# Optimization experiments

Measured on AMD Instinct MI355X. Metric: run time of the kernel, lower is better.

The kernel has to match this reference:

```python
import jax, jax.numpy as jnp
import numpy as np

VOCAB = 100000
EMB = 300
BATCH = 16384
TOTAL = 65536      # total ragged context tokens (avg 4 per instance)
NG_WORDS = 5


def setup_inputs() -> dict:
    key = jax.random.key(0)
    k1, k2, k3, k4, k5, k6 = jax.random.split(key, 6)
    # learned parameters: nn.Embedding weights, init uniform(-1, 1)
    W_in = jax.random.uniform(k1, (VOCAB, EMB), dtype=jnp.float32, minval=-1.0, maxval=1.0)
    W_out = jax.random.uniform(k2, (VOCAB, EMB), dtype=jnp.float32, minval=-1.0, maxval=1.0)
    # ragged batch flattened: indices + sorted segment ids (instance membership)
    flat_idx = jax.random.randint(k3, (TOTAL,), 0, VOCAB, dtype=jnp.int64)
    segment_ids = jnp.sort(jax.random.randint(k4, (TOTAL,), 0, BATCH, dtype=jnp.int64))
    out_idx = jax.random.randint(k5, (BATCH,), 0, VOCAB, dtype=jnp.int64)
    # forward_neg: multinomial over uniform dist == uniform randint over vocab
    ng_idx = jax.random.randint(k6, (BATCH * NG_WORDS,), 0, VOCAB, dtype=jnp.int64)
    return {"W_in": W_in, "W_out": W_out, "flat_idx": flat_idx,
            "segment_ids": segment_ids, "out_idx": out_idx, "ng_idx": ng_idx}


def reference(W_in, W_out, flat_idx, segment_ids, out_idx, ng_idx):
    # forward_in: per-instance sum of in-embedding rows (fused gather + segment_sum)
    in_vec = jax.ops.segment_sum(W_in[flat_idx], segment_ids, num_segments=BATCH)  # [B, EMB]
    # forward_out: plain embedding lookup
    out_vec = W_out[out_idx]                                                        # [B, EMB]
    # forward_neg: negative-sample embeddings, viewed [B, NG_WORDS, EMB]
    neg_vec = W_out[ng_idx].reshape(BATCH, NG_WORDS, EMB)
    return (in_vec, out_vec, neg_vec)
```

## Files before the change

kernel.cpp:

```cpp
#include <hip/hip_runtime.h>

#define VOCAB  100000
#define EMB    300
#define BATCH  16384
#define TOTAL  65536
#define NG     5
#define CHUNKS 75

__global__ __launch_bounds__(64) void segsum_kernel(
    const float* __restrict__ W_in,
    const int*   __restrict__ flat_idx,
    const int*   __restrict__ seg_ids,
    float*       __restrict__ in_vec)
{
    const int seg  = blockIdx.x;
    const int lane = threadIdx.x;

    int lo = 0, hi = TOTAL;
    while (lo < hi) { int mid = (lo + hi) >> 1; if (seg_ids[mid] < seg) lo = mid + 1; else hi = mid; }
    const int start = lo;
    hi = TOTAL;
    while (lo < hi) { int mid = (lo + hi) >> 1; if (seg_ids[mid] < seg + 1) lo = mid + 1; else hi = mid; }
    const int end = lo;

    float4 acc0 = make_float4(0.f, 0.f, 0.f, 0.f);
    float4 acc1 = make_float4(0.f, 0.f, 0.f, 0.f);
    const bool extra = lane < (CHUNKS - 64);

    for (int t = start; t < end; ++t) {
        const int idx = flat_idx[t];
        const float4* row = reinterpret_cast<const float4*>(W_in + (size_t)idx * EMB);
        const float4 v0 = row[lane];
        acc0.x += v0.x; acc0.y += v0.y; acc0.z += v0.z; acc0.w += v0.w;
        if (extra) {
            const float4 v1 = row[lane + 64];
            acc1.x += v1.x; acc1.y += v1.y; acc1.z += v1.z; acc1.w += v1.w;
        }
    }

    float4* dst = reinterpret_cast<float4*>(in_vec + (size_t)seg * EMB);
    dst[lane] = acc0;
    if (extra) dst[lane + 64] = acc1;
}

__global__ __launch_bounds__(256) void gather_kernel(
    const float* __restrict__ W_out,
    const int*   __restrict__ out_idx,
    const int*   __restrict__ ng_idx,
    float*       __restrict__ out_vec,
    float*       __restrict__ neg_vec)
{
    const int gid = blockIdx.x * blockDim.x + threadIdx.x;
    const int total_chunks = (BATCH + BATCH * NG) * CHUNKS;
    if (gid >= total_chunks) return;

    const int row = gid / CHUNKS;
    const int c   = gid % CHUNKS;

    int idx;
    float* dst;
    if (row < BATCH) {
        idx = out_idx[row];
        dst = out_vec + (size_t)row * EMB;
    } else {
        const int rr = row - BATCH;
        idx = ng_idx[rr];
        dst = neg_vec + (size_t)rr * EMB;
    }

    const float4* src = reinterpret_cast<const float4*>(W_out + (size_t)idx * EMB);
    reinterpret_cast<float4*>(dst)[c] = src[c];
}

extern "C" void kernel_launch(void* const* d_in, const int* in_sizes, int n_in,
                              void* d_out, int out_size, void* d_ws, size_t ws_size,
                              hipStream_t stream)
{
    const float* W_in   = (const float*)d_in[0];
    const float* W_out  = (const float*)d_in[1];
    const int*   flat   = (const int*)d_in[2];
    const int*   segids = (const int*)d_in[3];
    const int*   outidx = (const int*)d_in[4];
    const int*   ngidx  = (const int*)d_in[5];

    float* o       = (float*)d_out;
    float* in_vec  = o;
    float* out_vec = o + (size_t)BATCH * EMB;
    float* neg_vec = o + (size_t)2 * BATCH * EMB;

    segsum_kernel<<<BATCH, 64, 0, stream>>>(W_in, flat, segids, in_vec);

    const int total_chunks = (BATCH + BATCH * NG) * CHUNKS;
    const int threads = 256;
    const int blocks  = (total_chunks + threads - 1) / threads;
    gather_kernel<<<blocks, threads, 0, stream>>>(W_out, outidx, ngidx, out_vec, neg_vec);
}
```

Measured before the change: 73.01 us.

## Fuse segment-sum and gather into one interleaved kernel with ballot-based bounds search

Merges the segment-sum and the W_out gather into one launch. Every eighth block in the first span runs segment-sum work with four segments per block, and the other blocks copy gather chunks, so the two memory-bound workloads overlap on the device. The serial binary search is replaced by a three-level wavefront ballot search. Indices are loaded cooperatively and broadcast with shuffles, and outputs use nontemporal stores. This removes one launch and the serialized latency-bound search, at the cost of more complex block indexing and an uneven mix of work per block.

```diff
diff --git a/kernel.cpp b/kernel.cpp
--- a/kernel.cpp
+++ b/kernel.cpp
@@ -7,69 +7,90 @@
 #define NG     5
 #define CHUNKS 75
 
-__global__ __launch_bounds__(64) void segsum_kernel(
+#define NBLK_A 4096
+#define NBLK_B 28800
+#define NBLK   (NBLK_A + NBLK_B)
+#define A_SPAN (NBLK_A * 8)
+
+typedef float f4 __attribute__((ext_vector_type(4)));
+
+__device__ __forceinline__ int lb64(const int* __restrict__ seg, int v, int lane) {
+    int base = 0;
+    unsigned long long m;
+    int p = lane * 1024 + 1023;
+    m = __ballot(seg[p] < v);
+    base += (int)__popcll(m) << 10;
+    p = base + lane * 16 + 15;
+    m = __ballot((p < TOTAL) && (seg[p] < v));
+    base += (int)__popcll(m) << 4;
+    p = base + lane;
+    m = __ballot((lane < 16) && (p < TOTAL) && (seg[p] < v));
+    base += (int)__popcll(m);
+    return base;
+}
+
+__global__ __launch_bounds__(256) void fused_kernel(
     const float* __restrict__ W_in,
+    const float* __restrict__ W_out,
     const int*   __restrict__ flat_idx,
     const int*   __restrict__ seg_ids,
-    float*       __restrict__ in_vec)
-{
-    const int seg  = blockIdx.x;
-    const int lane = threadIdx.x;
-
-    int lo = 0, hi = TOTAL;
-    while (lo < hi) { int mid = (lo + hi) >> 1; if (seg_ids[mid] < seg) lo = mid + 1; else hi = mid; }
-    const int start = lo;
-    hi = TOTAL;
-    while (lo < hi) { int mid = (lo + hi) >> 1; if (seg_ids[mid] < seg + 1) lo = mid + 1; else hi = mid; }
-    const int end = lo;
-
-    float4 acc0 = make_float4(0.f, 0.f, 0.f, 0.f);
-    float4 acc1 = make_float4(0.f, 0.f, 0.f, 0.f);
-    const bool extra = lane < (CHUNKS - 64);
-
-    for (int t = start; t < end; ++t) {
-        const int idx = flat_idx[t];
-        const float4* row = reinterpret_cast<const float4*>(W_in + (size_t)idx * EMB);
-        const float4 v0 = row[lane];
-        acc0.x += v0.x; acc0.y += v0.y; acc0.z += v0.z; acc0.w += v0.w;
-        if (extra) {
-            const float4 v1 = row[lane + 64];
-            acc1.x += v1.x; acc1.y += v1.y; acc1.z += v1.z; acc1.w += v1.w;
-        }
-    }
-
-    float4* dst = reinterpret_cast<float4*>(in_vec + (size_t)seg * EMB);
-    dst[lane] = acc0;
-    if (extra) dst[lane + 64] = acc1;
-}
-
-__global__ __launch_bounds__(256) void gather_kernel(
-    const float* __restrict__ W_out,
     const int*   __restrict__ out_idx,
     const int*   __restrict__ ng_idx,
+    float*       __restrict__ in_vec,
     float*       __restrict__ out_vec,
     float*       __restrict__ neg_vec)
 {
-    const int gid = blockIdx.x * blockDim.x + threadIdx.x;
-    const int total_chunks = (BATCH + BATCH * NG) * CHUNKS;
-    if (gid >= total_chunks) return;
+    const unsigned bid = blockIdx.x;
 
-    const int row = gid / CHUNKS;
-    const int c   = gid % CHUNKS;
+    if (bid < A_SPAN && (bid & 7u) == 0u) {
+        const int aid  = (int)(bid >> 3);
+        const int wid  = threadIdx.x >> 6;
+        const int lane = threadIdx.x & 63;
+        const int seg  = aid * 4 + wid;
 
-    int idx;
-    float* dst;
-    if (row < BATCH) {
-        idx = out_idx[row];
-        dst = out_vec + (size_t)row * EMB;
+        const int start = lb64(seg_ids, seg,     lane);
+        const int end   = lb64(seg_ids, seg + 1, lane);
+
+        f4 acc0 = {0.f, 0.f, 0.f, 0.f};
+        f4 acc1 = {0.f, 0.f, 0.f, 0.f};
+        const bool extra = lane < (CHUNKS - 64);
+
+        for (int t0 = start; t0 < end; t0 += 64) {
+            const int n = min(64, end - t0);
+            const int myidx = (lane < n) ? flat_idx[t0 + lane] : 0;
+            for (int j = 0; j < n; ++j) {
+                const int idx = __shfl(myidx, j);
+                const f4* row = reinterpret_cast<const f4*>(W_in + (size_t)idx * EMB);
+                acc0 += row[lane];
+                if (extra) acc1 += row[lane + 64];
+            }
+        }
+
+        f4* dst = reinterpret_cast<f4*>(in_vec + (size_t)seg * EMB);
+        __builtin_nontemporal_store(acc0, dst + lane);
+        if (extra) __builtin_nontemporal_store(acc1, dst + lane + 64);
     } else {
-        const int rr = row - BATCH;
-        idx = ng_idx[rr];
-        dst = neg_vec + (size_t)rr * EMB;
+        const int b = (bid < A_SPAN) ? (int)(bid - (bid >> 3) - 1u)
+                                     : (int)(NBLK_A * 7 + (bid - A_SPAN));
+        const int gid = b * 256 + (int)threadIdx.x;
+        const int row = gid / CHUNKS;
+        const int c   = gid - row * CHUNKS;
+
+        int idx;
+        float* dstbase;
+        if (row < BATCH) {
+            idx = out_idx[row];
+            dstbase = out_vec + (size_t)row * EMB;
+        } else {
+            const int rr = row - BATCH;
+            idx = ng_idx[rr];
+            dstbase = neg_vec + (size_t)rr * EMB;
+        }
+
+        const f4* src = reinterpret_cast<const f4*>(W_out + (size_t)idx * EMB);
+        const f4 v = src[c];
+        __builtin_nontemporal_store(v, reinterpret_cast<f4*>(dstbase) + c);
     }
-
-    const float4* src = reinterpret_cast<const float4*>(W_out + (size_t)idx * EMB);
-    reinterpret_cast<float4*>(dst)[c] = src[c];
 }
 
 extern "C" void kernel_launch(void* const* d_in, const int* in_sizes, int n_in,
@@ -88,10 +109,6 @@
     float* out_vec = o + (size_t)BATCH * EMB;
     float* neg_vec = o + (size_t)2 * BATCH * EMB;
 
-    segsum_kernel<<<BATCH, 64, 0, stream>>>(W_in, flat, segids, in_vec);
-
-    const int total_chunks = (BATCH + BATCH * NG) * CHUNKS;
-    const int threads = 256;
-    const int blocks  = (total_chunks + threads - 1) / threads;
-    gather_kernel<<<blocks, threads, 0, stream>>>(W_out, outidx, ngidx, out_vec, neg_vec);
+    fused_kernel<<<NBLK, 256, 0, stream>>>(W_in, W_out, flat, segids,
+                                           outidx, ngidx, in_vec, out_vec, neg_vec);
 }
```

Result: slower. 107.5 us (+47.2%).
